# Performance work log

Hardware: AMD Instinct MI355X
Metric: run time of the kernel (lower is better)

The kernel has to match this reference:

```python
import jax, jax.numpy as jnp
import numpy as np

R = 4
SCALING = 2.0  # lora_alpha / r = 2r/r
NUM_EXPERTS = 3
TOP_K = 1
EPS = 1e-6
C = 64
DW = 128   # c * DW_Expand
FFN = 128  # c * FFN_Expand
B, H, W = 4, 256, 256
K3 = 3


def _conv(x, w, groups, pad):
    return jax.lax.conv_general_dilated(
        x, w, (1, 1), [(pad, pad), (pad, pad)],
        dimension_numbers=('NCHW', 'OIHW', 'NCHW'),
        feature_group_count=groups)


def conv2dmix(x, w, b, la, lb, gate, groups, pad):
    # base conv + top-k gated mixture of LoRA expert deltas (conv is linear in w)
    out = _conv(x, w, groups, pad) + b[None, :, None, None]
    for e in range(NUM_EXPERTS):
        dw = (lb[e] @ la[e]).reshape(w.shape) * SCALING  # low-rank delta weight
        out = out + gate[:, e][:, None, None, None] * _conv(x, dw, groups, pad)
    return out


def ln2d(x, w, b):
    mu = jnp.mean(x, axis=1, keepdims=True)
    var = jnp.var(x, axis=1, keepdims=True)
    return (x - mu) / jnp.sqrt(var + EPS) * w[None, :, None, None] + b[None, :, None, None]


def simple_gate(x):
    x1, x2 = jnp.split(x, 2, axis=1)
    return x1 * x2


def setup_inputs() -> dict:
    key = jax.random.key(0)
    ks = list(jax.random.split(key, 40))
    k = iter(ks)
    rn = lambda shape, s=0.05: jax.random.normal(next(k), shape, dtype=jnp.float32) * s
    d = {}
    d['inp'] = jax.random.normal(next(k), (B, C, H, W), dtype=jnp.float32)
    d['probs'] = jax.random.uniform(next(k), (B, NUM_EXPERTS), dtype=jnp.float32)
    d['ln1_w'] = jnp.ones((C,), jnp.float32); d['ln1_b'] = jnp.zeros((C,), jnp.float32)
    d['ln2_w'] = jnp.ones((C,), jnp.float32); d['ln2_b'] = jnp.zeros((C,), jnp.float32)
    # conv1: 1x1, C -> DW
    d['w1'] = rn((DW, C, 1, 1)); d['b1'] = jnp.zeros((DW,), jnp.float32)
    d['la1'] = rn((NUM_EXPERTS, R, C)); d['lb1'] = rn((NUM_EXPERTS, DW, R))
    # conv2: 3x3 depthwise, DW -> DW, groups=DW  (loralib ConvLoRA shapes)
    d['w2'] = rn((DW, 1, K3, K3)); d['b2'] = jnp.zeros((DW,), jnp.float32)
    d['la2'] = rn((NUM_EXPERTS, R * K3, 1 * K3)); d['lb2'] = rn((NUM_EXPERTS, DW * K3, R * K3))
    # sca conv: 1x1, DW//2 -> DW//2
    d['wsca'] = rn((DW // 2, DW // 2, 1, 1)); d['bsca'] = jnp.zeros((DW // 2,), jnp.float32)
    d['lasca'] = rn((NUM_EXPERTS, R, DW // 2)); d['lbsca'] = rn((NUM_EXPERTS, DW // 2, R))
    # conv3: 1x1, DW//2 -> C
    d['w3'] = rn((C, DW // 2, 1, 1)); d['b3'] = jnp.zeros((C,), jnp.float32)
    d['la3'] = rn((NUM_EXPERTS, R, DW // 2)); d['lb3'] = rn((NUM_EXPERTS, C, R))
    # conv4: 1x1, C -> FFN
    d['w4'] = rn((FFN, C, 1, 1)); d['b4'] = jnp.zeros((FFN,), jnp.float32)
    d['la4'] = rn((NUM_EXPERTS, R, C)); d['lb4'] = rn((NUM_EXPERTS, FFN, R))
    # conv5: 1x1, FFN//2 -> C
    d['w5'] = rn((C, FFN // 2, 1, 1)); d['b5'] = jnp.zeros((C,), jnp.float32)
    d['la5'] = rn((NUM_EXPERTS, R, FFN // 2)); d['lb5'] = rn((NUM_EXPERTS, C, R))
    d['beta'] = jnp.zeros((1, C, 1, 1), jnp.float32) + 0.1
    d['gamma'] = jnp.zeros((1, C, 1, 1), jnp.float32) + 0.1
    return d


def reference(inp, probs, ln1_w, ln1_b, ln2_w, ln2_b,
              w1, b1, la1, lb1, w2, b2, la2, lb2,
              wsca, bsca, lasca, lbsca, w3, b3, la3, lb3,
              w4, b4, la4, lb4, w5, b5, la5, lb5, beta, gamma):
    # top-k gate per sample: keep top_k probs, zero the rest (no renorm)
    vals, idx = jax.lax.top_k(probs, TOP_K)
    gate = jnp.zeros_like(probs).at[jnp.arange(probs.shape[0])[:, None], idx].set(vals)

    x = ln2d(inp, ln1_w, ln1_b)
    x = conv2dmix(x, w1, b1, la1, lb1, gate, 1, 0)
    x = conv2dmix(x, w2, b2, la2, lb2, gate, DW, 1)
    x = simple_gate(x)
    pooled = jnp.mean(x, axis=(2, 3), keepdims=True)
    x = x * conv2dmix(pooled, wsca, bsca, lasca, lbsca, gate, 1, 0)
    x = conv2dmix(x, w3, b3, la3, lb3, gate, 1, 0)
    y = inp + x * beta
    x = conv2dmix(ln2d(y, ln2_w, ln2_b), w4, b4, la4, lb4, gate, 1, 0)
    x = simple_gate(x)
    x = conv2dmix(x, w5, b5, la5, lb5, gate, 1, 0)
    return y + x * gamma
```

## Files before the change

### kernel.cpp

```cpp
#include <hip/hip_runtime.h>
#include <hip/hip_bf16.h>

#define HW 65536
#define WST 29952

typedef unsigned short U16;
typedef __attribute__((ext_vector_type(8))) short short8;
typedef __attribute__((ext_vector_type(4))) unsigned short us4;
typedef __attribute__((ext_vector_type(4))) float float4v;

#define WEFF_OFF 0
#define FRAG_OFF 524288
#define POOL_OFF 786432
#define SCA_OFF  787456
#define T1_OFF   1048576
#define Z_OFF    68157440

__device__ inline U16 f2bf(float f) {
  union { float f; unsigned u; } v; v.f = f;
  unsigned r = v.u + 0x7FFF + ((v.u >> 16) & 1);
  return (U16)(r >> 16);
}
__device__ inline float bf2f(U16 h) {
  union { unsigned u; float f; } v; v.u = ((unsigned)h) << 16;
  return v.f;
}
__device__ inline float asfhi(unsigned u) {
  union { unsigned u; float f; } v; v.u = u & 0xffff0000u; return v.f;
}
__device__ inline float asflo(unsigned u) {
  union { unsigned u; float f; } v; v.u = u << 16; return v.f;
}

__global__ __launch_bounds__(256) void k_weights(const float* __restrict__ probs,
    const float* __restrict__ w1, const float* __restrict__ la1, const float* __restrict__ lb1,
    const float* __restrict__ w2, const float* __restrict__ la2, const float* __restrict__ lb2,
    const float* __restrict__ wsca, const float* __restrict__ lasca, const float* __restrict__ lbsca,
    const float* __restrict__ w3, const float* __restrict__ la3, const float* __restrict__ lb3,
    const float* __restrict__ w4, const float* __restrict__ la4, const float* __restrict__ lb4,
    const float* __restrict__ w5, const float* __restrict__ la5, const float* __restrict__ lb5,
    const float* __restrict__ b3, const float* __restrict__ b5,
    const float* __restrict__ beta, const float* __restrict__ gamma,
    float* __restrict__ weff, U16* __restrict__ fragw)
{
  __shared__ float sb[4992];
  int blk = blockIdx.x;
  int b = blk / 6, sec = blk - b * 6;
  int tid = threadIdx.x;
  float p0 = probs[b*3+0], p1 = probs[b*3+1], p2 = probs[b*3+2];
  int e = 0; float g = p0;
  if (p1 > g) { g = p1; e = 1; }
  if (p2 > g) { g = p2; e = 2; }
  float s = 2.0f * g;
  float* wfp = weff + b * WST;
  U16* fws = fragw + b * 24576;

  if (sec == 1) {
    const float* lbs = lb2 + e * 4608;
    const float* las = la2 + e * 36;
    for (int i = tid; i < 4608; i += 256) sb[i] = lbs[i];
    if (tid < 36) sb[4608 + tid] = las[tid];
    if (tid < 64) {
      sb[4644 + tid] = b3[tid];  sb[4708 + tid] = b5[tid];
      sb[4772 + tid] = beta[tid]; sb[4836 + tid] = gamma[tid];
    }
    __syncthreads();
    for (int idx = tid; idx < 1152; idx += 256) {
      int row = idx / 3, dx = idx - row * 3;
      float acc = w2[idx];
      #pragma unroll
      for (int r = 0; r < 12; ++r)
        acc += s * sb[row*12 + r] * sb[4608 + r*3 + dx];
      wfp[8192 + idx] = acc;
    }
    if (tid < 64) {
      wfp[29824 + tid] = sb[4644 + tid] * sb[4772 + tid];
      wfp[29888 + tid] = sb[4708 + tid] * sb[4836 + tid];
    }
    return;
  }
  if (sec == 2) {
    const float* lbs = lbsca + e * 256;
    const float* las = lasca + e * 256;
    if (tid < 256) { sb[tid] = lbs[tid]; sb[256 + tid] = las[tid]; }
    __syncthreads();
    #pragma unroll 4
    for (int idx = tid; idx < 4096; idx += 256) {
      int c = idx >> 6, k = idx & 63;
      float acc = wsca[k*64 + c];
      #pragma unroll
      for (int r = 0; r < 4; ++r)
        acc += s * sb[k*4 + r] * sb[256 + r*64 + c];
      wfp[9344 + idx] = acc;
    }
    return;
  }

  const float *w, *la, *lb, *scl = nullptr;
  int fo, cnt;
  if (sec == 0)      { w = w1; lb = lb1 + e*512; la = la1 + e*256; fo = 0;     cnt = 8192; }
  else if (sec == 3) { w = w3; lb = lb3 + e*256; la = la3 + e*256; fo = 8192;  cnt = 4096; scl = beta; }
  else if (sec == 4) { w = w4; lb = lb4 + e*512; la = la4 + e*256; fo = 12288; cnt = 8192; }
  else               { w = w5; lb = lb5 + e*256; la = la5 + e*256; fo = 20480; cnt = 4096; scl = gamma; }
  int nlb = (cnt == 8192) ? 512 : 256;
  for (int i = tid; i < nlb; i += 256) sb[i] = lb[i];
  if (tid < 256) sb[512 + tid] = la[tid];
  if (scl && tid < 64) sb[768 + tid] = scl[tid];
  __syncthreads();
  #pragma unroll 4
  for (int idx = tid; idx < cnt; idx += 256) {
    int j = idx & 7, l = (idx >> 3) & 63, s2 = (idx >> 9) & 1, nt = idx >> 10;
    int n = nt*16 + (l & 15), k = s2*32 + ((l >> 4) << 3) + j;
    float acc = w[n*64 + k];
    #pragma unroll
    for (int r = 0; r < 4; ++r)
      acc += s * sb[n*4 + r] * sb[512 + r*64 + k];
    if (scl) acc *= sb[768 + n];
    fws[fo + idx] = f2bf(acc);
  }
}

__global__ __launch_bounds__(256, 2) void k_conv1(
    const float* __restrict__ inp, const float* __restrict__ ln1w, const float* __restrict__ ln1b,
    const float* __restrict__ b1, const U16* __restrict__ fragw, U16* __restrict__ t1)
{
  __shared__ __align__(16) U16 sm[16640];
  int blk = blockIdx.x;
  int b = blk >> 8, h = blk & 255;
  int tid = threadIdx.x, lane = tid & 63, w = tid >> 6;

  {
    const float* src = inp + (size_t)b*64*HW + h*256 + tid;
    float x[64];
    #pragma unroll
    for (int c = 0; c < 64; ++c) x[c] = src[(size_t)c * HW];
    float s0=0,s1=0,q0=0,q1=0;
    #pragma unroll
    for (int c = 0; c < 64; c += 2) {
      s0 += x[c];   q0 += x[c]*x[c];
      s1 += x[c+1]; q1 += x[c+1]*x[c+1];
    }
    float mu  = (s0+s1) * (1.f/64.f);
    float inv = rsqrtf((q0+q1) * (1.f/64.f) - mu*mu + 1e-6f);
    #pragma unroll
    for (int c = 0; c < 64; ++c) x[c] = (x[c] - mu) * inv * ln1w[c] + ln1b[c];
    int mt = tid >> 4, m = tid & 15;
    #pragma unroll
    for (int s = 0; s < 2; ++s)
      #pragma unroll
      for (int q = 0; q < 4; ++q) {
        short8 v;
        #pragma unroll
        for (int j = 0; j < 8; ++j) v[j] = (short)f2bf(x[s*32 + q*8 + j]);
        *(short8*)&sm[mt*1024 + s*512 + (q*16 + m)*8] = v;
      }
  }
  __syncthreads();

  const U16* fw = fragw + b * 24576;
  short8 bw[16];
  #pragma unroll
  for (int i = 0; i < 16; ++i) bw[i] = *(const short8*)&fw[(i*64 + lane)*8];
  float4v acc[4][8];
  #pragma unroll
  for (int mi = 0; mi < 4; ++mi)
    #pragma unroll
    for (int nt = 0; nt < 8; ++nt) acc[mi][nt] = (float4v)(0.f);
  #pragma unroll
  for (int mi = 0; mi < 4; ++mi) {
    int mt = w*4 + mi;
    #pragma unroll
    for (int s = 0; s < 2; ++s) {
      short8 a = *(const short8*)&sm[mt*1024 + s*512 + lane*8];
      #pragma unroll
      for (int nt = 0; nt < 8; ++nt)
        acc[mi][nt] = __builtin_amdgcn_mfma_f32_16x16x32_bf16(a, bw[nt*2 + s], acc[mi][nt], 0, 0, 0);
    }
  }
  float b1v[8];
  #pragma unroll
  for (int nt = 0; nt < 8; ++nt) b1v[nt] = b1[nt*16 + (lane & 15)];
  __syncthreads();

  for (int half = 0; half < 2; ++half) {
    if (half) __syncthreads();
    #pragma unroll
    for (int mi = 0; mi < 4; ++mi) {
      int px0 = (w*4 + mi)*16 + ((lane >> 4) << 2);
      #pragma unroll
      for (int nt2 = 0; nt2 < 4; ++nt2) {
        int nt = half*4 + nt2;
        int jr = nt2*16 + (lane & 15);
        us4 pk;
        #pragma unroll
        for (int r = 0; r < 4; ++r) pk[r] = f2bf(acc[mi][nt][r] + b1v[nt]);
        *(us4*)&sm[jr*260 + px0] = pk;
      }
    }
    __syncthreads();
    U16* dst = t1 + ((size_t)(b*128 + half*64)) * HW + h*256;
    #pragma unroll 4
    for (int it = 0; it < 32; ++it) {
      int idx = it*256 + tid;
      int jr = idx >> 7, pp2 = (idx & 127) * 2;
      *(unsigned*)&dst[(size_t)jr * HW + pp2] = *(unsigned*)&sm[jr*260 + pp2];
    }
  }
}

__global__ __launch_bounds__(256) void k_dwgate(
    const U16* __restrict__ t1, const float* __restrict__ weff, const float* __restrict__ b2,
    U16* __restrict__ z)
{
  int blk = blockIdx.x;
  int kg = blk & 3;
  int hp = (blk >> 2) & 127;
  int b  = blk >> 9;
  int tid = threadIdx.x;
  int h = hp*2 + (tid >> 7);
  int px0 = (tid & 127) * 2;
  const float* w2e = weff + b*WST + 8192;
  const U16* tbase = t1 + (size_t)b*128*HW + (size_t)h*256 + px0;
  U16* zb = z + (size_t)b*64*HW + (size_t)h*256 + px0;
  bool okm = px0 > 0, okp = px0 < 254;
  bool ok0 = h > 0, ok2 = h < 255;

  #pragma unroll 2
  for (int kk = 0; kk < 16; ++kk) {
    int k = kg*16 + kk;
    const U16* ta = tbase + (size_t)k * HW;
    const U16* tc = ta + (size_t)64 * HW;
    unsigned La[9], Lc[9];
    #pragma unroll
    for (int dy = 0; dy < 3; ++dy) {
      bool okr = (dy == 0) ? ok0 : (dy == 2 ? ok2 : true);
      int ro = (dy - 1) * 256;
      La[dy*3+0] = (okr && okm) ? *(const unsigned*)(ta + ro - 2) : 0u;
      La[dy*3+1] =  okr         ? *(const unsigned*)(ta + ro)     : 0u;
      La[dy*3+2] = (okr && okp) ? *(const unsigned*)(ta + ro + 2) : 0u;
    }
    #pragma unroll
    for (int dy = 0; dy < 3; ++dy) {
      bool okr = (dy == 0) ? ok0 : (dy == 2 ? ok2 : true);
      int ro = (dy - 1) * 256;
      Lc[dy*3+0] = (okr && okm) ? *(const unsigned*)(tc + ro - 2) : 0u;
      Lc[dy*3+1] =  okr         ? *(const unsigned*)(tc + ro)     : 0u;
      Lc[dy*3+2] = (okr && okp) ? *(const unsigned*)(tc + ro + 2) : 0u;
    }
    const float* wa = w2e + k*9;
    const float* wc = w2e + (k+64)*9;
    float a0 = b2[k], a1 = a0;
    float c0 = b2[k+64], c1 = c0;
    #pragma unroll
    for (int dy = 0; dy < 3; ++dy) {
      float xm1 = asfhi(La[dy*3+0]), x0 = asflo(La[dy*3+1]);
      float x1  = asfhi(La[dy*3+1]), x2 = asflo(La[dy*3+2]);
      a0 += wa[dy*3]*xm1 + wa[dy*3+1]*x0 + wa[dy*3+2]*x1;
      a1 += wa[dy*3]*x0  + wa[dy*3+1]*x1 + wa[dy*3+2]*x2;
      xm1 = asfhi(Lc[dy*3+0]); x0 = asflo(Lc[dy*3+1]);
      x1  = asfhi(Lc[dy*3+1]); x2 = asflo(Lc[dy*3+2]);
      c0 += wc[dy*3]*xm1 + wc[dy*3+1]*x0 + wc[dy*3+2]*x1;
      c1 += wc[dy*3]*x0  + wc[dy*3+1]*x1 + wc[dy*3+2]*x2;
    }
    unsigned pz = (unsigned)f2bf(a0*c0) | ((unsigned)f2bf(a1*c1) << 16);
    *(unsigned*)(zb + (size_t)k * HW) = pz;
  }
}

__global__ void k_pool(const U16* __restrict__ z, float* __restrict__ pooled)
{
  __shared__ float red[256];
  int b = blockIdx.x >> 6, k = blockIdx.x & 63;
  int tid = threadIdx.x;
  const unsigned* zp = (const unsigned*)(z + ((size_t)(b*64 + k)) * HW);
  float s = 0.f;
  for (int it = 0; it < 128; ++it) {
    unsigned u = zp[it*256 + tid];
    s += asflo(u) + asfhi(u);
  }
  red[tid] = s;
  __syncthreads();
  for (int st = 128; st >= 1; st >>= 1) {
    if (tid < st) red[tid] += red[tid + st];
    __syncthreads();
  }
  if (tid == 0) pooled[b*64 + k] = red[0];
}

__global__ void k_sca(const float* __restrict__ bsca, const float* __restrict__ weff,
                      const float* __restrict__ pooled, float* __restrict__ sca)
{
  int b = blockIdx.x, k = threadIdx.x;
  const float* wt = weff + b * WST + 9344;
  const float* pm = pooled + b * 64;
  float acc = bsca[k];
  for (int c = 0; c < 64; ++c) acc += wt[c * 64 + k] * (pm[c] * (1.f/65536.f));
  sca[b * 64 + k] = acc;
}

__global__ __launch_bounds__(256, 2) void k_stage2(
    const float* __restrict__ inp, const U16* __restrict__ z, const float* __restrict__ sca,
    const float* __restrict__ ln2w, const float* __restrict__ ln2b, const float* __restrict__ b4,
    const float* __restrict__ weff, const U16* __restrict__ fragw, float* __restrict__ out)
{
  __shared__ __align__(16) U16 yb[256*72];
  __shared__ __align__(16) char afr[34816];
  U16* afrag = (U16*)afr;
  float* afragF = (float*)afr;
  int blk = blockIdx.x;
  int b = blk >> 8, h = blk & 255;
  int tid = threadIdx.x, lane = tid & 63, w = tid >> 6;
  const float* wb = weff + b * WST;
  const U16* fw = fragw + b * 24576;

  float y0[64];
  {
    const U16* zp = z + (size_t)b*64*HW + h*256 + tid;
    const float* scb = sca + b*64;
    float xs[64];
    #pragma unroll
    for (int k = 0; k < 64; ++k) xs[k] = bf2f(zp[(size_t)k * HW]) * scb[k];
    int mt = tid >> 4, m = tid & 15;
    #pragma unroll
    for (int s = 0; s < 2; ++s)
      #pragma unroll
      for (int q = 0; q < 4; ++q) {
        short8 v;
        #pragma unroll
        for (int j = 0; j < 8; ++j) v[j] = (short)f2bf(xs[s*32 + q*8 + j]);
        *(short8*)&afrag[mt*1024 + s*512 + (q*16 + m)*8] = v;
      }
    const float* ip = inp + (size_t)b*64*HW + h*256 + tid;
    #pragma unroll
    for (int c = 0; c < 64; ++c) y0[c] = ip[(size_t)c * HW];
  }
  __syncthreads();

  {
    short8 bw3[8];
    #pragma unroll
    for (int i = 0; i < 8; ++i) bw3[i] = *(const short8*)&fw[8192 + (i*64 + lane)*8];
    float4v acc[4][4];
    #pragma unroll
    for (int mi = 0; mi < 4; ++mi)
      #pragma unroll
      for (int nt = 0; nt < 4; ++nt) acc[mi][nt] = (float4v)(0.f);
    #pragma unroll
    for (int mi = 0; mi < 4; ++mi) {
      int mt = w*4 + mi;
      #pragma unroll
      for (int s = 0; s < 2; ++s) {
        short8 a = *(const short8*)&afrag[mt*1024 + s*512 + lane*8];
        #pragma unroll
        for (int nt = 0; nt < 4; ++nt)
          acc[mi][nt] = __builtin_amdgcn_mfma_f32_16x16x32_bf16(a, bw3[nt*2 + s], acc[mi][nt], 0, 0, 0);
      }
    }
    #pragma unroll
    for (int mi = 0; mi < 4; ++mi) {
      int pxb = (w*4 + mi)*16 + ((lane >> 4) << 2);
      #pragma unroll
      for (int nt = 0; nt < 4; ++nt) {
        int c = nt*16 + (lane & 15);
        #pragma unroll
        for (int r = 0; r < 4; ++r)
          yb[(pxb + r)*72 + c] = f2bf(acc[mi][nt][r]);
      }
    }
  }
  __syncthreads();

  {
    const float* b3b = wb + 29824;
    float y[64];
    #pragma unroll
    for (int c8 = 0; c8 < 8; ++c8) {
      short8 v = *(const short8*)&yb[tid*72 + c8*8];
      #pragma unroll
      for (int j = 0; j < 8; ++j) y[c8*8 + j] = bf2f((U16)v[j]);
    }
    #pragma unroll
    for (int c = 0; c < 64; ++c) y[c] += y0[c] + b3b[c];
    float s0=0,s1=0,q0=0,q1=0;
    #pragma unroll
    for (int c = 0; c < 64; c += 2) {
      s0 += y[c];   q0 += y[c]*y[c];
      s1 += y[c+1]; q1 += y[c+1]*y[c+1];
    }
    float mu  = (s0+s1) * (1.f/64.f);
    float inv = rsqrtf((q0+q1) * (1.f/64.f) - mu*mu + 1e-6f);
    int mt = tid >> 4, m = tid & 15;
    #pragma unroll
    for (int s = 0; s < 2; ++s)
      #pragma unroll
      for (int q = 0; q < 4; ++q) {
        short8 v;
        #pragma unroll
        for (int j = 0; j < 8; ++j) {
          int c = s*32 + q*8 + j;
          v[j] = (short)f2bf((y[c] - mu) * inv * ln2w[c] + ln2b[c]);
        }
        *(short8*)&afrag[mt*1024 + s*512 + (q*16 + m)*8] = v;
      }
    #pragma unroll
    for (int c8 = 0; c8 < 8; ++c8) {
      short8 v;
      #pragma unroll
      for (int j = 0; j < 8; ++j) v[j] = (short)f2bf(y[c8*8 + j]);
      *(short8*)&yb[tid*72 + c8*8] = v;
    }
  }
  __syncthreads();

  float4v acc5[4][4];
  {
    short8 bw4[16];
    #pragma unroll
    for (int i = 0; i < 16; ++i) bw4[i] = *(const short8*)&fw[12288 + (i*64 + lane)*8];
    float b4a[8];
    #pragma unroll
    for (int nt = 0; nt < 8; ++nt) b4a[nt] = b4[nt*16 + (lane & 15)];
    float4v acc[4][8];
    #pragma unroll
    for (int mi = 0; mi < 4; ++mi)
      #pragma unroll
      for (int nt = 0; nt < 8; ++nt) acc[mi][nt] = (float4v)(0.f);
    #pragma unroll
    for (int mi = 0; mi < 4; ++mi) {
      int mt = w*4 + mi;
      #pragma unroll
      for (int s = 0; s < 2; ++s) {
        short8 a = *(const short8*)&afrag[mt*1024 + s*512 + lane*8];
        #pragma unroll
        for (int nt = 0; nt < 8; ++nt)
          acc[mi][nt] = __builtin_amdgcn_mfma_f32_16x16x32_bf16(a, bw4[nt*2 + s], acc[mi][nt], 0, 0, 0);
      }
    }
    #pragma unroll
    for (int mi = 0; mi < 4; ++mi) {
      int mt = w*4 + mi;
      int mloc = ((lane >> 4) << 2);
      #pragma unroll
      for (int nt = 0; nt < 4; ++nt) {
        int k = nt*16 + (lane & 15);
        int s_ = k >> 5, q = (k >> 3) & 3, j = k & 7;
        #pragma unroll
        for (int r = 0; r < 4; ++r) {
          float gv = (acc[mi][nt][r] + b4a[nt]) * (acc[mi][nt+4][r] + b4a[nt+4]);
          afrag[mt*1024 + s_*512 + (q*16 + mloc + r)*8 + j] = f2bf(gv);
        }
      }
    }
    short8 bw5[8];
    #pragma unroll
    for (int i = 0; i < 8; ++i) bw5[i] = *(const short8*)&fw[20480 + (i*64 + lane)*8];
    #pragma unroll
    for (int mi = 0; mi < 4; ++mi)
      #pragma unroll
      for (int nt = 0; nt < 4; ++nt) acc5[mi][nt] = (float4v)(0.f);
    #pragma unroll
    for (int mi = 0; mi < 4; ++mi) {
      int mt = w*4 + mi;
      #pragma unroll
      for (int s = 0; s < 2; ++s) {
        short8 a = *(const short8*)&afrag[mt*1024 + s*512 + lane*8];
        #pragma unroll
        for (int nt = 0; nt < 4; ++nt)
          acc5[mi][nt] = __builtin_amdgcn_mfma_f32_16x16x32_bf16(a, bw5[nt*2 + s], acc5[mi][nt], 0, 0, 0);
      }
    }
  }
  __syncthreads();

  {
    const float* b5g = wb + 29888;
    float b5f[4];
    #pragma unroll
    for (int nt = 0; nt < 4; ++nt) b5f[nt] = b5g[nt*16 + (lane & 15)];
    float* op = out + (size_t)b*64*HW + h*256;
    for (int chalf = 0; chalf < 2; ++chalf) {
      #pragma unroll
      for (int mi = 0; mi < 4; ++mi) {
        int pxb = (w*4 + mi)*16 + ((lane >> 4) << 2);
        #pragma unroll
        for (int nt2 = 0; nt2 < 2; ++nt2) {
          int nt = chalf*2 + nt2;
          int c = nt*16 + (lane & 15);
          #pragma unroll
          for (int r = 0; r < 4; ++r) {
            float v = acc5[mi][nt][r] + b5f[nt] + bf2f(yb[(pxb + r)*72 + c]);
            afragF[(pxb + r)*33 + (c - chalf*32)] = v;
          }
        }
      }
      #pragma unroll 4
      for (int cc = 0; cc < 32; ++cc)
        op[(size_t)(chalf*32 + cc) * HW + tid] = afragF[tid*33 + cc];
    }
  }
}

extern "C" void kernel_launch(void* const* d_in, const int* in_sizes, int n_in,
                              void* d_out, int out_size, void* d_ws, size_t ws_size,
                              hipStream_t stream) {
  const float* inp   = (const float*)d_in[0];
  const float* probs = (const float*)d_in[1];
  const float* ln1w  = (const float*)d_in[2];
  const float* ln1b  = (const float*)d_in[3];
  const float* ln2w  = (const float*)d_in[4];
  const float* ln2b  = (const float*)d_in[5];
  const float* w1    = (const float*)d_in[6];
  const float* b1    = (const float*)d_in[7];
  const float* la1   = (const float*)d_in[8];
  const float* lb1   = (const float*)d_in[9];
  const float* w2    = (const float*)d_in[10];
  const float* b2    = (const float*)d_in[11];
  const float* la2   = (const float*)d_in[12];
  const float* lb2   = (const float*)d_in[13];
  const float* wsca  = (const float*)d_in[14];
  const float* bsca  = (const float*)d_in[15];
  const float* lasca = (const float*)d_in[16];
  const float* lbsca = (const float*)d_in[17];
  const float* w3    = (const float*)d_in[18];
  const float* b3    = (const float*)d_in[19];
  const float* la3   = (const float*)d_in[20];
  const float* lb3   = (const float*)d_in[21];
  const float* w4    = (const float*)d_in[22];
  const float* b4    = (const float*)d_in[23];
  const float* la4   = (const float*)d_in[24];
  const float* lb4   = (const float*)d_in[25];
  const float* w5    = (const float*)d_in[26];
  const float* b5    = (const float*)d_in[27];
  const float* la5   = (const float*)d_in[28];
  const float* lb5   = (const float*)d_in[29];
  const float* beta  = (const float*)d_in[30];
  const float* gamma = (const float*)d_in[31];

  char* wsb = (char*)d_ws;
  float* weff   = (float*)(wsb + WEFF_OFF);
  U16*   fragw  = (U16*)(wsb + FRAG_OFF);
  float* pooled = (float*)(wsb + POOL_OFF);
  float* scap   = (float*)(wsb + SCA_OFF);
  U16*   t1     = (U16*)(wsb + T1_OFF);
  U16*   zws    = (U16*)(wsb + Z_OFF);
  float* outp   = (float*)d_out;

  k_weights<<<dim3(24), dim3(256), 0, stream>>>(probs,
      w1, la1, lb1, w2, la2, lb2, wsca, lasca, lbsca,
      w3, la3, lb3, w4, la4, lb4, w5, la5, lb5,
      b3, b5, beta, gamma, weff, fragw);
  k_conv1<<<dim3(1024), dim3(256), 0, stream>>>(inp, ln1w, ln1b, b1, fragw, t1);
  k_dwgate<<<dim3(2048), dim3(256), 0, stream>>>(t1, weff, b2, zws);
  k_pool<<<dim3(256), dim3(256), 0, stream>>>(zws, pooled);
  k_sca<<<dim3(4), dim3(64), 0, stream>>>(bsca, weff, pooled, scap);
  k_stage2<<<dim3(1024), dim3(256), 0, stream>>>(inp, zws, scap, ln2w, ln2b, b4, weff, fragw, outp);
}
```

Before: 292.7 us.

## Fuse LN1, conv1, depthwise gate and pooling into one tiled kernel

```diff
diff --git a/kernel.cpp b/kernel.cpp
--- a/kernel.cpp
+++ b/kernel.cpp
@@ -13,7 +13,6 @@
 #define FRAG_OFF 524288
 #define POOL_OFF 786432
 #define SCA_OFF  787456
-#define T1_OFF   1048576
 #define Z_OFF    68157440
 
 __device__ inline U16 f2bf(float f) {
@@ -41,9 +40,10 @@
     const float* __restrict__ w5, const float* __restrict__ la5, const float* __restrict__ lb5,
     const float* __restrict__ b3, const float* __restrict__ b5,
     const float* __restrict__ beta, const float* __restrict__ gamma,
+    const float* __restrict__ ln1w, const float* __restrict__ ln1b, const float* __restrict__ b1,
     float* __restrict__ weff, U16* __restrict__ fragw)
 {
-  __shared__ float sb[4992];
+  __shared__ float sb[5952];
   int blk = blockIdx.x;
   int b = blk / 6, sec = blk - b * 6;
   int tid = threadIdx.x;
@@ -63,7 +63,11 @@
     if (tid < 64) {
       sb[4644 + tid] = b3[tid];  sb[4708 + tid] = b5[tid];
       sb[4772 + tid] = beta[tid]; sb[4836 + tid] = gamma[tid];
-    }
+      sb[5668 + tid] = ln1w[tid]; sb[5732 + tid] = ln1b[tid];
+    }
+    if (tid < 256) sb[4900 + tid] = la1[e*256 + tid];
+    for (int i = tid; i < 512; i += 256) sb[5156 + i] = lb1[e*512 + i];
+    if (tid < 128) sb[5796 + tid] = b1[tid];
     __syncthreads();
     for (int idx = tid; idx < 1152; idx += 256) {
       int row = idx / 3, dx = idx - row * 3;
@@ -76,6 +80,18 @@
     if (tid < 64) {
       wfp[29824 + tid] = sb[4644 + tid] * sb[4772 + tid];
       wfp[29888 + tid] = sb[4708 + tid] * sb[4836 + tid];
+    }
+    if (tid >= 128) {
+      int n = tid - 128;
+      float S = 0.f, Bn = sb[5796 + n];
+      for (int c = 0; c < 64; ++c) {
+        float wv = w1[n*64 + c];
+        #pragma unroll
+        for (int r = 0; r < 4; ++r) wv += s * sb[5156 + n*4 + r] * sb[4900 + r*64 + c];
+        S  += bf2f(f2bf(wv * sb[5668 + c]));
+        Bn += wv * sb[5732 + c];
+      }
+      wfp[n] = S; wfp[128 + n] = Bn;
     }
     return;
   }
@@ -97,8 +113,9 @@
   }
 
   const float *w, *la, *lb, *scl = nullptr;
+  bool sclk = false;
   int fo, cnt;
-  if (sec == 0)      { w = w1; lb = lb1 + e*512; la = la1 + e*256; fo = 0;     cnt = 8192; }
+  if (sec == 0)      { w = w1; lb = lb1 + e*512; la = la1 + e*256; fo = 0;     cnt = 8192; scl = ln1w; sclk = true; }
   else if (sec == 3) { w = w3; lb = lb3 + e*256; la = la3 + e*256; fo = 8192;  cnt = 4096; scl = beta; }
   else if (sec == 4) { w = w4; lb = lb4 + e*512; la = la4 + e*256; fo = 12288; cnt = 8192; }
   else               { w = w5; lb = lb5 + e*256; la = la5 + e*256; fo = 20480; cnt = 4096; scl = gamma; }
@@ -115,176 +132,171 @@
     #pragma unroll
     for (int r = 0; r < 4; ++r)
       acc += s * sb[n*4 + r] * sb[512 + r*64 + k];
-    if (scl) acc *= sb[768 + n];
+    if (scl) acc *= sb[768 + (sclk ? k : n)];
     fws[fo + idx] = f2bf(acc);
   }
 }
 
-__global__ __launch_bounds__(256, 2) void k_conv1(
-    const float* __restrict__ inp, const float* __restrict__ ln1w, const float* __restrict__ ln1b,
-    const float* __restrict__ b1, const U16* __restrict__ fragw, U16* __restrict__ t1)
+#define MTS 22
+__global__ __launch_bounds__(256, 3) void k_stage1f(
+    const float* __restrict__ inp, const float* __restrict__ b2,
+    const float* __restrict__ weff, const U16* __restrict__ fragw,
+    U16* __restrict__ z, float* __restrict__ pooled)
 {
-  __shared__ __align__(16) U16 sm[16640];
+  __shared__ __align__(16) U16 smu[22528];
+  __shared__ float2 muinv[344];
+  __shared__ float poolbuf[4][16];
   int blk = blockIdx.x;
-  int b = blk >> 8, h = blk & 255;
+  int tile = blk & 255;
+  int g = (blk >> 8) & 1;
+  int b = blk >> 9;
+  int h0 = (tile >> 3) * 8, w0 = (tile & 7) * 32;
   int tid = threadIdx.x, lane = tid & 63, w = tid >> 6;
+  const float* wfp = weff + b * WST;
+  const U16* fw = fragw + b * 24576;
+
+  for (int it = 0; it < 2; ++it) {
+    int i = tid + it * 256;
+    if (i >= 340) break;
+    int hy = i / 34, hx = i - hy * 34;
+    int h = h0 - 1 + hy, ww = w0 - 1 + hx;
+    int mt = i >> 4, m = i & 15;
+    if (h >= 0 && h < 256 && ww >= 0 && ww < 256) {
+      const float* src = inp + (size_t)b * 64 * HW + h * 256 + ww;
+      float x[64];
+      #pragma unroll
+      for (int c = 0; c < 64; ++c) x[c] = src[(size_t)c * HW];
+      float s0=0,s1=0,q0=0,q1=0;
+      #pragma unroll
+      for (int c = 0; c < 64; c += 2) {
+        s0 += x[c];   q0 += x[c]*x[c];
+        s1 += x[c+1]; q1 += x[c+1]*x[c+1];
+      }
+      float mu  = (s0+s1) * (1.f/64.f);
+      float inv = rsqrtf(fmaxf((q0+q1)*(1.f/64.f) - mu*mu, 0.f) + 1e-6f);
+      muinv[i] = float2{mu, inv};
+      #pragma unroll
+      for (int s = 0; s < 2; ++s)
+        #pragma unroll
+        for (int q = 0; q < 4; ++q) {
+          short8 v;
+          #pragma unroll
+          for (int j = 0; j < 8; ++j) v[j] = (short)f2bf(x[s*32 + q*8 + j]);
+          *(short8*)&smu[mt*1024 + s*512 + (q*16 + m)*8] = v;
+        }
+    } else {
+      muinv[i] = float2{0.f, 0.f};
+    }
+  }
+
+  int n15 = lane & 15;
+  short8 bw[8];
+  float Sr[4], Br[4];
+  #pragma unroll
+  for (int ntl = 0; ntl < 4; ++ntl) {
+    int ntg = (ntl < 2) ? (g*2 + ntl) : (4 + g*2 + (ntl - 2));
+    #pragma unroll
+    for (int s = 0; s < 2; ++s)
+      bw[ntl*2 + s] = *(const short8*)&fw[((ntg*2 + s)*64 + lane)*8];
+    int ng = ntg*16 + n15;
+    Sr[ntl] = wfp[ng];
+    Br[ntl] = wfp[128 + ng];
+  }
+  __syncthreads();
+
+  int mt0 = w * 6;
+  int nmt = MTS - mt0; if (nmt > 6) nmt = 6;
+  float4v acc[6][4];
+  #pragma unroll
+  for (int mi = 0; mi < 6; ++mi)
+    #pragma unroll
+    for (int ntl = 0; ntl < 4; ++ntl) acc[mi][ntl] = (float4v)(0.f);
+  #pragma unroll
+  for (int mi = 0; mi < 6; ++mi) {
+    if (mi < nmt) {
+      int mt = mt0 + mi;
+      #pragma unroll
+      for (int s = 0; s < 2; ++s) {
+        short8 a = *(const short8*)&smu[mt*1024 + s*512 + lane*8];
+        #pragma unroll
+        for (int ntl = 0; ntl < 4; ++ntl)
+          acc[mi][ntl] = __builtin_amdgcn_mfma_f32_16x16x32_bf16(a, bw[ntl*2 + s], acc[mi][ntl], 0, 0, 0);
+      }
+    }
+  }
+  __syncthreads();
+
+  int q = lane >> 4;
+  #pragma unroll
+  for (int mi = 0; mi < 6; ++mi) {
+    if (mi < nmt) {
+      int px0 = (mt0 + mi)*16 + q*4;
+      if (px0 < 340) {
+        float2 m0 = muinv[px0], m1 = muinv[px0+1], m2 = muinv[px0+2], m3 = muinv[px0+3];
+        #pragma unroll
+        for (int ntl = 0; ntl < 4; ++ntl) {
+          float S = Sr[ntl], B = Br[ntl];
+          us4 pk;
+          float v0 = m0.y*(acc[mi][ntl][0] - m0.x*S) + B;
+          float v1 = m1.y*(acc[mi][ntl][1] - m1.x*S) + B;
+          float v2 = m2.y*(acc[mi][ntl][2] - m2.x*S) + B;
+          float v3 = m3.y*(acc[mi][ntl][3] - m3.x*S) + B;
+          pk[0] = f2bf(m0.y > 0.f ? v0 : 0.f);
+          pk[1] = f2bf(m1.y > 0.f ? v1 : 0.f);
+          pk[2] = f2bf(m2.y > 0.f ? v2 : 0.f);
+          pk[3] = f2bf(m3.y > 0.f ? v3 : 0.f);
+          *(us4*)&smu[(ntl*16 + n15)*348 + px0] = pk;
+        }
+      }
+    }
+  }
+  __syncthreads();
 
   {
-    const float* src = inp + (size_t)b*64*HW + h*256 + tid;
-    float x[64];
-    #pragma unroll
-    for (int c = 0; c < 64; ++c) x[c] = src[(size_t)c * HW];
-    float s0=0,s1=0,q0=0,q1=0;
-    #pragma unroll
-    for (int c = 0; c < 64; c += 2) {
-      s0 += x[c];   q0 += x[c]*x[c];
-      s1 += x[c+1]; q1 += x[c+1]*x[c+1];
-    }
-    float mu  = (s0+s1) * (1.f/64.f);
-    float inv = rsqrtf((q0+q1) * (1.f/64.f) - mu*mu + 1e-6f);
-    #pragma unroll
-    for (int c = 0; c < 64; ++c) x[c] = (x[c] - mu) * inv * ln1w[c] + ln1b[c];
-    int mt = tid >> 4, m = tid & 15;
-    #pragma unroll
-    for (int s = 0; s < 2; ++s)
-      #pragma unroll
-      for (int q = 0; q < 4; ++q) {
-        short8 v;
-        #pragma unroll
-        for (int j = 0; j < 8; ++j) v[j] = (short)f2bf(x[s*32 + q*8 + j]);
-        *(short8*)&sm[mt*1024 + s*512 + (q*16 + m)*8] = v;
-      }
-  }
-  __syncthreads();
-
-  const U16* fw = fragw + b * 24576;
-  short8 bw[16];
-  #pragma unroll
-  for (int i = 0; i < 16; ++i) bw[i] = *(const short8*)&fw[(i*64 + lane)*8];
-  float4v acc[4][8];
-  #pragma unroll
-  for (int mi = 0; mi < 4; ++mi)
-    #pragma unroll
-    for (int nt = 0; nt < 8; ++nt) acc[mi][nt] = (float4v)(0.f);
-  #pragma unroll
-  for (int mi = 0; mi < 4; ++mi) {
-    int mt = w*4 + mi;
-    #pragma unroll
-    for (int s = 0; s < 2; ++s) {
-      short8 a = *(const short8*)&sm[mt*1024 + s*512 + lane*8];
-      #pragma unroll
-      for (int nt = 0; nt < 8; ++nt)
-        acc[mi][nt] = __builtin_amdgcn_mfma_f32_16x16x32_bf16(a, bw[nt*2 + s], acc[mi][nt], 0, 0, 0);
-    }
-  }
-  float b1v[8];
-  #pragma unroll
-  for (int nt = 0; nt < 8; ++nt) b1v[nt] = b1[nt*16 + (lane & 15)];
-  __syncthreads();
-
-  for (int half = 0; half < 2; ++half) {
-    if (half) __syncthreads();
-    #pragma unroll
-    for (int mi = 0; mi < 4; ++mi) {
-      int px0 = (w*4 + mi)*16 + ((lane >> 4) << 2);
-      #pragma unroll
-      for (int nt2 = 0; nt2 < 4; ++nt2) {
-        int nt = half*4 + nt2;
-        int jr = nt2*16 + (lane & 15);
-        us4 pk;
-        #pragma unroll
-        for (int r = 0; r < 4; ++r) pk[r] = f2bf(acc[mi][nt][r] + b1v[nt]);
-        *(us4*)&sm[jr*260 + px0] = pk;
-      }
-    }
-    __syncthreads();
-    U16* dst = t1 + ((size_t)(b*128 + half*64)) * HW + h*256;
-    #pragma unroll 4
-    for (int it = 0; it < 32; ++it) {
-      int idx = it*256 + tid;
-      int jr = idx >> 7, pp2 = (idx & 127) * 2;
-      *(unsigned*)&dst[(size_t)jr * HW + pp2] = *(unsigned*)&sm[jr*260 + pp2];
-    }
-  }
-}
-
-__global__ __launch_bounds__(256) void k_dwgate(
-    const U16* __restrict__ t1, const float* __restrict__ weff, const float* __restrict__ b2,
-    U16* __restrict__ z)
-{
-  int blk = blockIdx.x;
-  int kg = blk & 3;
-  int hp = (blk >> 2) & 127;
-  int b  = blk >> 9;
-  int tid = threadIdx.x;
-  int h = hp*2 + (tid >> 7);
-  int px0 = (tid & 127) * 2;
-  const float* w2e = weff + b*WST + 8192;
-  const U16* tbase = t1 + (size_t)b*128*HW + (size_t)h*256 + px0;
-  U16* zb = z + (size_t)b*64*HW + (size_t)h*256 + px0;
-  bool okm = px0 > 0, okp = px0 < 254;
-  bool ok0 = h > 0, ok2 = h < 255;
-
-  #pragma unroll 2
-  for (int kk = 0; kk < 16; ++kk) {
-    int k = kg*16 + kk;
-    const U16* ta = tbase + (size_t)k * HW;
-    const U16* tc = ta + (size_t)64 * HW;
-    unsigned La[9], Lc[9];
-    #pragma unroll
-    for (int dy = 0; dy < 3; ++dy) {
-      bool okr = (dy == 0) ? ok0 : (dy == 2 ? ok2 : true);
-      int ro = (dy - 1) * 256;
-      La[dy*3+0] = (okr && okm) ? *(const unsigned*)(ta + ro - 2) : 0u;
-      La[dy*3+1] =  okr         ? *(const unsigned*)(ta + ro)     : 0u;
-      La[dy*3+2] = (okr && okp) ? *(const unsigned*)(ta + ro + 2) : 0u;
-    }
-    #pragma unroll
-    for (int dy = 0; dy < 3; ++dy) {
-      bool okr = (dy == 0) ? ok0 : (dy == 2 ? ok2 : true);
-      int ro = (dy - 1) * 256;
-      Lc[dy*3+0] = (okr && okm) ? *(const unsigned*)(tc + ro - 2) : 0u;
-      Lc[dy*3+1] =  okr         ? *(const unsigned*)(tc + ro)     : 0u;
-      Lc[dy*3+2] = (okr && okp) ? *(const unsigned*)(tc + ro + 2) : 0u;
-    }
-    const float* wa = w2e + k*9;
-    const float* wc = w2e + (k+64)*9;
-    float a0 = b2[k], a1 = a0;
-    float c0 = b2[k+64], c1 = c0;
-    #pragma unroll
-    for (int dy = 0; dy < 3; ++dy) {
-      float xm1 = asfhi(La[dy*3+0]), x0 = asflo(La[dy*3+1]);
-      float x1  = asfhi(La[dy*3+1]), x2 = asflo(La[dy*3+2]);
-      a0 += wa[dy*3]*xm1 + wa[dy*3+1]*x0 + wa[dy*3+2]*x1;
-      a1 += wa[dy*3]*x0  + wa[dy*3+1]*x1 + wa[dy*3+2]*x2;
-      xm1 = asfhi(Lc[dy*3+0]); x0 = asflo(Lc[dy*3+1]);
-      x1  = asfhi(Lc[dy*3+1]); x2 = asflo(Lc[dy*3+2]);
-      c0 += wc[dy*3]*xm1 + wc[dy*3+1]*x0 + wc[dy*3+2]*x1;
-      c1 += wc[dy*3]*x0  + wc[dy*3+1]*x1 + wc[dy*3+2]*x2;
-    }
-    unsigned pz = (unsigned)f2bf(a0*c0) | ((unsigned)f2bf(a1*c1) << 16);
-    *(unsigned*)(zb + (size_t)k * HW) = pz;
-  }
-}
-
-__global__ void k_pool(const U16* __restrict__ z, float* __restrict__ pooled)
-{
-  __shared__ float red[256];
-  int b = blockIdx.x >> 6, k = blockIdx.x & 63;
-  int tid = threadIdx.x;
-  const unsigned* zp = (const unsigned*)(z + ((size_t)(b*64 + k)) * HW);
-  float s = 0.f;
-  for (int it = 0; it < 128; ++it) {
-    unsigned u = zp[it*256 + tid];
-    s += asflo(u) + asfhi(u);
-  }
-  red[tid] = s;
-  __syncthreads();
-  for (int st = 128; st >= 1; st >>= 1) {
-    if (tid < st) red[tid] += red[tid + st];
-    __syncthreads();
-  }
-  if (tid == 0) pooled[b*64 + k] = red[0];
+    int half = tid >> 7;
+    int pp = (tid & 127) * 2;
+    int cy = pp >> 5, cx = pp & 31;
+    const float* w2e = wfp + 8192;
+    U16* zb = z + (size_t)b*64*HW + (size_t)(h0 + cy)*256 + (w0 + cx);
+    #pragma unroll 2
+    for (int i = 0; i < 16; ++i) {
+      int kl = half*16 + i;
+      int kg = g*32 + kl;
+      unsigned ua[3][2], uc[3][2];
+      #pragma unroll
+      for (int dy = 0; dy < 3; ++dy) {
+        int basea = kl*348 + (cy + dy)*34 + cx;
+        int basec = (32 + kl)*348 + (cy + dy)*34 + cx;
+        ua[dy][0] = *(unsigned*)&smu[basea]; ua[dy][1] = *(unsigned*)&smu[basea + 2];
+        uc[dy][0] = *(unsigned*)&smu[basec]; uc[dy][1] = *(unsigned*)&smu[basec + 2];
+      }
+      const float* wa = w2e + kg*9;
+      const float* wc = w2e + (kg + 64)*9;
+      float a0 = b2[kg], a1 = a0;
+      float c0 = b2[kg + 64], c1 = c0;
+      #pragma unroll
+      for (int dy = 0; dy < 3; ++dy) {
+        float x0 = asflo(ua[dy][0]), x1 = asfhi(ua[dy][0]), x2 = asflo(ua[dy][1]), x3 = asfhi(ua[dy][1]);
+        a0 += wa[dy*3]*x0 + wa[dy*3+1]*x1 + wa[dy*3+2]*x2;
+        a1 += wa[dy*3]*x1 + wa[dy*3+1]*x2 + wa[dy*3+2]*x3;
+        x0 = asflo(uc[dy][0]); x1 = asfhi(uc[dy][0]); x2 = asflo(uc[dy][1]); x3 = asfhi(uc[dy][1]);
+        c0 += wc[dy*3]*x0 + wc[dy*3+1]*x1 + wc[dy*3+2]*x2;
+        c1 += wc[dy*3]*x1 + wc[dy*3+1]*x2 + wc[dy*3+2]*x3;
+      }
+      float z0 = a0*c0, z1 = a1*c1;
+      *(unsigned*)(zb + (size_t)kg * HW) = (unsigned)f2bf(z0) | ((unsigned)f2bf(z1) << 16);
+      float ps = z0 + z1;
+      #pragma unroll
+      for (int off = 32; off >= 1; off >>= 1) ps += __shfl_down(ps, off, 64);
+      if (lane == 0) poolbuf[w][i] = ps;
+    }
+  }
+  __syncthreads();
+  if (tid < 32) {
+    float v = (tid < 16) ? (poolbuf[0][tid] + poolbuf[1][tid])
+                         : (poolbuf[2][tid - 16] + poolbuf[3][tid - 16]);
+    atomicAdd(&pooled[b*64 + g*32 + tid], v);
+  }
 }
 
 __global__ void k_sca(const float* __restrict__ bsca, const float* __restrict__ weff,
@@ -541,17 +553,15 @@
   U16*   fragw  = (U16*)(wsb + FRAG_OFF);
   float* pooled = (float*)(wsb + POOL_OFF);
   float* scap   = (float*)(wsb + SCA_OFF);
-  U16*   t1     = (U16*)(wsb + T1_OFF);
   U16*   zws    = (U16*)(wsb + Z_OFF);
   float* outp   = (float*)d_out;
 
+  hipMemsetAsync(pooled, 0, 256 * sizeof(float), stream);
   k_weights<<<dim3(24), dim3(256), 0, stream>>>(probs,
       w1, la1, lb1, w2, la2, lb2, wsca, lasca, lbsca,
       w3, la3, lb3, w4, la4, lb4, w5, la5, lb5,
-      b3, b5, beta, gamma, weff, fragw);
-  k_conv1<<<dim3(1024), dim3(256), 0, stream>>>(inp, ln1w, ln1b, b1, fragw, t1);
-  k_dwgate<<<dim3(2048), dim3(256), 0, stream>>>(t1, weff, b2, zws);
-  k_pool<<<dim3(256), dim3(256), 0, stream>>>(zws, pooled);
+      b3, b5, beta, gamma, ln1w, ln1b, b1, weff, fragw);
+  k_stage1f<<<dim3(2048), dim3(256), 0, stream>>>(inp, b2, weff, fragw, zws, pooled);
   k_sca<<<dim3(4), dim3(64), 0, stream>>>(bsca, weff, pooled, scap);
   k_stage2<<<dim3(1024), dim3(256), 0, stream>>>(inp, zws, scap, ln2w, ln2b, b4, weff, fragw, outp);
 }
```

New measurement: 289.7 us. Within noise of the previous version (-1.0%).
